# Optimization experiments

Hardware: AMD Instinct MI355X
Metric: run time of the kernel (lower is better)

Reference implementation:

```python
import jax, jax.numpy as jnp
import numpy as np

BS9 = 9
NA9 = BS9 * BS9  # 81


def _make_windows():
    """All 5-in-a-row windows on a 9x9 board, as flat cell indices. (140, 5)."""
    wins = []
    for dr, dc in ((0, 1), (1, 0), (1, 1), (1, -1)):
        for r in range(BS9):
            for c in range(BS9):
                er, ec = r + 4 * dr, c + 4 * dc
                if 0 <= er < BS9 and 0 <= ec < BS9:
                    wins.append([(r + k * dr) * BS9 + (c + k * dc) for k in range(5)])
    return np.asarray(wins, dtype=np.int32)

_W_NP = _make_windows()                      # (140, 5)
_M_NP = np.zeros((NA9, _W_NP.shape[0]), dtype=np.int32)
for w in range(_W_NP.shape[0]):
    _M_NP[_W_NP[w], w] = 1                   # MEMBER[idx, w] = 1 iff cell idx is in window w

WINDOWS = jnp.asarray(_W_NP)                 # (140, 5)
MEMBER = jnp.asarray(_M_NP)                  # (81, 140)
# score table indexed by stone count 0..5 (pc>=5 clamps to 5 since window len is 5)
TABLE = jnp.asarray([0.0, 5.0, 50.0, 500.0, 5000.0, 100000.0], dtype=jnp.float32)


def setup_inputs() -> dict:
    key = jax.random.key(0)
    k1, k2 = jax.random.split(key)
    B = 2048
    boards = jax.random.randint(k1, (B, NA9), 0, 3).astype(jnp.float32)   # cells in {0,1,2}
    current_player = jax.random.randint(k2, (B,), 1, 3).astype(jnp.int32) # {1,2}
    return {"boards": boards, "current_player": current_player}


def reference(boards, current_player):
    # boards: (B, 81) float32 with values {0,1,2}; current_player: (B,) int32 {1,2}
    player = current_player.astype(boards.dtype)[:, None, None]  # (B,1,1)
    opp = 3.0 - player
    cells = boards[:, WINDOWS]                                    # (B,140,5)
    pc = jnp.sum(cells == player, axis=-1)                        # (B,140) player count per window
    oc = jnp.sum(cells == opp, axis=-1)                           # (B,140) opponent count

    # static eval of the current board (used for the value head)
    plus = jnp.where((oc == 0) & (pc > 0), TABLE[pc], 0.0)
    minus = jnp.where((pc == 0) & (oc > 0), TABLE[oc], 0.0)
    ev = jnp.sum(plus - minus, axis=-1)                           # (B,)

    # 1-ply lookahead: placing player's stone at empty cell idx adds MEMBER[idx] to pc
    pc_new = pc[:, None, :] + MEMBER[None]                        # (B,81,140)
    win = jnp.any((MEMBER[None] == 1) & (pc_new == 5), axis=-1)   # (B,81)
    ocb = oc[:, None, :]
    plus_n = jnp.where((ocb == 0) & (pc_new > 0), TABLE[pc_new], 0.0)
    minus_n = jnp.where((pc_new == 0) & (ocb > 0), TABLE[ocb], 0.0)
    score = jnp.sum(plus_n - minus_n, axis=-1)                    # (B,81)

    empty = boards == 0                                           # (B,81)
    logits = jnp.where(empty, jnp.where(win, 100000.0, score), -1000000.0)
    policy = jax.nn.softmax(logits * 0.03, axis=-1)               # (B,81)
    value = jnp.clip(jnp.tanh(ev / 3000.0), -0.95, 0.95)[:, None] # (B,1)
    return policy, value
```

## Files before the change

kernel.cpp:

```cpp
#include <hip/hip_runtime.h>
#include <math.h>

#define NB 81
#define NW 140

struct Tables {
    unsigned long long mlo[NW];
    unsigned long long mhi[NW];
    unsigned cw32[NB][5];
};

constexpr Tables make_tables() {
    Tables t{};
    for (int a = 0; a < NB; ++a)
        for (int j = 0; j < 5; ++j) t.cw32[a][j] = 0x8C8C8C8Cu;
    int cnt[NB] = {};
    const int DR[4] = {0, 1, 1, 1};
    const int DC[4] = {1, 0, 1, -1};
    int w = 0;
    for (int d = 0; d < 4; ++d)
        for (int r = 0; r < 9; ++r)
            for (int c = 0; c < 9; ++c) {
                const int er = r + 4 * DR[d], ec = c + 4 * DC[d];
                if (er < 0 || er > 8 || ec < 0 || ec > 8) continue;
                unsigned long long lo = 0, hi = 0;
                for (int k = 0; k < 5; ++k) {
                    const int cell = (r + k * DR[d]) * 9 + (c + k * DC[d]);
                    if (cell < 64) lo |= 1ull << cell;
                    else           hi |= 1ull << (cell - 64);
                    const int i = cnt[cell]++;
                    t.cw32[cell][i >> 2] &= ~(0xFFu << (8 * (i & 3)));
                    t.cw32[cell][i >> 2] |= (unsigned)w << (8 * (i & 3));
                }
                t.mlo[w] = lo; t.mhi[w] = hi; ++w;
            }
    return t;
}

__device__ __constant__ Tables TAB = make_tables();
__device__ __constant__ float PT[6] = {0.f, 5.f, 50.f, 500.f, 5000.f, 100000.f};
__device__ __constant__ float DT[6] = {5.f, 45.f, 450.f, 4500.f, 95000.f, 0.f};

__device__ __forceinline__ float wave_sum(float v) {
#pragma unroll
    for (int m = 1; m < 64; m <<= 1) v += __shfl_xor(v, m, 64);
    return v;
}
__device__ __forceinline__ float wave_max(float v) {
#pragma unroll
    for (int m = 1; m < 64; m <<= 1) v = fmaxf(v, __shfl_xor(v, m, 64));
    return v;
}

__global__ __launch_bounds__(256) void heur9_kernel(const float* __restrict__ boards,
                                                    const int* __restrict__ cur,
                                                    float* __restrict__ out, int B) {
    __shared__ float sD[4][NW + 1];
    const int wave = threadIdx.x >> 6;
    const int lane = threadIdx.x & 63;
    const int b = (blockIdx.x << 2) | wave;
    float* dl = sD[wave];
    const float* brd = boards + b * NB;

    const float pf = (float)cur[b];
    const float of = 3.0f - pf;
    const float v1 = brd[lane];
    const float v2 = (lane < NB - 64) ? brd[lane + 64] : -1.0f;

    const unsigned long long p_lo = __ballot(v1 == pf);
    const unsigned long long p_hi = __ballot((lane < NB - 64) && v2 == pf);
    const unsigned long long o_lo = __ballot(v1 == of);
    const unsigned long long o_hi = __ballot((lane < NB - 64) && v2 == of);
    const unsigned long long e_lo = ~(p_lo | o_lo);
    const unsigned long long e_hi = ~(p_hi | o_hi);

    float evp = 0.f;
    for (int w = lane; w < NW; w += 64) {
        const int pc = __popcll(p_lo & TAB.mlo[w]) + __popcll(p_hi & TAB.mhi[w]);
        const int oc = __popcll(o_lo & TAB.mlo[w]) + __popcll(o_hi & TAB.mhi[w]);
        float d = 0.f;
        if (oc == 0)      { d = DT[pc]; evp += PT[pc]; }
        else if (pc == 0) { d = PT[oc]; evp -= PT[oc]; }
        if (pc == 4) d = 1.0e9f;
        dl[w] = d;
    }
    if (lane == 0) dl[NW] = 0.f;
    const float ev = wave_sum(evp);
    __syncthreads();

    float sd1 = 0.f, sd2 = 0.f;
#pragma unroll
    for (int j = 0; j < 5; ++j) {
        const unsigned q = TAB.cw32[lane][j];
        sd1 += dl[q & 255] + dl[(q >> 8) & 255] + dl[(q >> 16) & 255] + dl[q >> 24];
    }
    if (lane < NB - 64) {
#pragma unroll
        for (int j = 0; j < 5; ++j) {
            const unsigned q = TAB.cw32[lane + 64][j];
            sd2 += dl[q & 255] + dl[(q >> 8) & 255] + dl[(q >> 16) & 255] + dl[q >> 24];
        }
    }
    const bool emp1 = (e_lo >> lane) & 1ull;
    const bool emp2 = (lane < NB - 64) && ((e_hi >> lane) & 1ull);
    float l1 = emp1 ? (sd1 >= 5.0e8f ? 100000.f : ev + sd1) : -1000000.f;
    float l2 = (lane < NB - 64)
                 ? (emp2 ? (sd2 >= 5.0e8f ? 100000.f : ev + sd2) : -1000000.f)
                 : -INFINITY;
    l1 *= 0.03f; l2 *= 0.03f;

    const float m = wave_max(fmaxf(l1, l2));
    const float e1 = __expf(l1 - m);
    const float e2 = (lane < NB - 64) ? __expf(l2 - m) : 0.f;
    const float inv = 1.0f / wave_sum(e1 + e2);

    out[b * NB + lane] = e1 * inv;
    if (lane < NB - 64) out[b * NB + lane + 64] = e2 * inv;
    if (lane == 0) {
        const float v = tanhf(ev * (1.f / 3000.f));
        out[B * NB + b] = fminf(fmaxf(v, -0.95f), 0.95f);
    }
}

extern "C" void kernel_launch(void* const* d_in, const int* in_sizes, int n_in,
                              void* d_out, int out_size, void* d_ws, size_t ws_size,
                              hipStream_t stream) {
    const float* boards = (const float*)d_in[0];
    const int* cur = (const int*)d_in[1];
    float* out = (float*)d_out;
    const int B = in_sizes[0] / NB;
    heur9_kernel<<<B / 4, 256, 0, stream>>>(boards, cur, out, B);
}
```

Before: 57.75 us.

## Replace per-cell window gathers with per-line prefix sums over window deltas

Groups the 140 windows into 36 board lines and has each line lane compute a running prefix sum of window deltas in shared memory. Each cell's lookahead score then becomes four prefix-sum differences (one per direction) instead of gathering up to 20 window deltas. This cuts shared-memory reads per cell but serialises a 5-step scan on only 36 lanes. It also lowers the win sentinel to 2^21 so float prefix differences stay exact, which relies on the non-win deltas staying well below the 1e6 threshold.

```diff
diff --git a/kernel.cpp b/kernel.cpp
--- a/kernel.cpp
+++ b/kernel.cpp
@@ -3,37 +3,59 @@
 
 #define NB 81
 #define NW 140
+#define NL 36
+#define PSZ (NL * 6)
+#define WINM 2097152.0f
 
 struct Tables {
-    unsigned long long mlo[NW];
-    unsigned long long mhi[NW];
-    unsigned cw32[NB][5];
+    unsigned long long lmlo[NL][5];
+    unsigned long long lmhi[NL][5];
+    unsigned char len[NL];
+    unsigned cellPS[NB][2];
 };
 
 constexpr Tables make_tables() {
     Tables t{};
+    int minp[NB][4] = {}, maxp[NB][4] = {}, lofc[NB][4] = {};
     for (int a = 0; a < NB; ++a)
-        for (int j = 0; j < 5; ++j) t.cw32[a][j] = 0x8C8C8C8Cu;
-    int cnt[NB] = {};
+        for (int d = 0; d < 4; ++d) { minp[a][d] = 99; maxp[a][d] = -1; }
     const int DR[4] = {0, 1, 1, 1};
     const int DC[4] = {1, 0, 1, -1};
-    int w = 0;
     for (int d = 0; d < 4; ++d)
         for (int r = 0; r < 9; ++r)
             for (int c = 0; c < 9; ++c) {
                 const int er = r + 4 * DR[d], ec = c + 4 * DC[d];
                 if (er < 0 || er > 8 || ec < 0 || ec > 8) continue;
+                int l = 0;
+                if (d == 0) l = r;
+                else if (d == 1) l = 9 + c;
+                else if (d == 2) l = 18 + (r - c + 4);
+                else l = 27 + (r + c - 4);
+                const int pos = t.len[l]++;
                 unsigned long long lo = 0, hi = 0;
                 for (int k = 0; k < 5; ++k) {
                     const int cell = (r + k * DR[d]) * 9 + (c + k * DC[d]);
                     if (cell < 64) lo |= 1ull << cell;
                     else           hi |= 1ull << (cell - 64);
-                    const int i = cnt[cell]++;
-                    t.cw32[cell][i >> 2] &= ~(0xFFu << (8 * (i & 3)));
-                    t.cw32[cell][i >> 2] |= (unsigned)w << (8 * (i & 3));
+                    lofc[cell][d] = l;
+                    if (pos < minp[cell][d]) minp[cell][d] = pos;
+                    if (pos > maxp[cell][d]) maxp[cell][d] = pos;
                 }
-                t.mlo[w] = lo; t.mhi[w] = hi; ++w;
+                t.lmlo[l][pos] = lo; t.lmhi[l][pos] = hi;
             }
+    for (int a = 0; a < NB; ++a) {
+        unsigned q[2] = {0, 0};
+        for (int d = 0; d < 4; ++d) {
+            unsigned hiS = 0, loS = 0;
+            if (maxp[a][d] >= 0) {
+                const int l = lofc[a][d];
+                loS = (unsigned)(l * 6 + minp[a][d]);
+                hiS = (unsigned)(l * 6 + 1 + maxp[a][d]);
+            }
+            q[d >> 1] |= (hiS | (loS << 8)) << (16 * (d & 1));
+        }
+        t.cellPS[a][0] = q[0]; t.cellPS[a][1] = q[1];
+    }
     return t;
 }
 
@@ -55,11 +77,11 @@
 __global__ __launch_bounds__(256) void heur9_kernel(const float* __restrict__ boards,
                                                     const int* __restrict__ cur,
                                                     float* __restrict__ out, int B) {
-    __shared__ float sD[4][NW + 1];
+    __shared__ float sP[4][PSZ];
     const int wave = threadIdx.x >> 6;
     const int lane = threadIdx.x & 63;
     const int b = (blockIdx.x << 2) | wave;
-    float* dl = sD[wave];
+    float* P = sP[wave];
     const float* brd = boards + b * NB;
 
     const float pf = (float)cur[b];
@@ -75,37 +97,42 @@
     const unsigned long long e_hi = ~(p_hi | o_hi);
 
     float evp = 0.f;
-    for (int w = lane; w < NW; w += 64) {
-        const int pc = __popcll(p_lo & TAB.mlo[w]) + __popcll(p_hi & TAB.mhi[w]);
-        const int oc = __popcll(o_lo & TAB.mlo[w]) + __popcll(o_hi & TAB.mhi[w]);
-        float d = 0.f;
-        if (oc == 0)      { d = DT[pc]; evp += PT[pc]; }
-        else if (pc == 0) { d = PT[oc]; evp -= PT[oc]; }
-        if (pc == 4) d = 1.0e9f;
-        dl[w] = d;
+    if (lane < NL) {
+        const int len = TAB.len[lane];
+        float run = 0.f;
+        P[lane * 6] = 0.f;
+#pragma unroll
+        for (int pos = 0; pos < 5; ++pos) {
+            const unsigned long long ml = TAB.lmlo[lane][pos];
+            const unsigned long long mh = TAB.lmhi[lane][pos];
+            const int pc = __popcll(p_lo & ml) + __popcll(p_hi & mh);
+            const int oc = __popcll(o_lo & ml) + __popcll(o_hi & mh);
+            float d = 0.f;
+            if (oc == 0)      { d = DT[pc]; evp += PT[pc]; }
+            else if (pc == 0) { d = PT[oc]; evp -= PT[oc]; }
+            if (pc == 4) d = WINM;
+            if (pos >= len) d = 0.f;
+            run += d;
+            P[lane * 6 + 1 + pos] = run;
+        }
     }
-    if (lane == 0) dl[NW] = 0.f;
     const float ev = wave_sum(evp);
     __syncthreads();
 
-    float sd1 = 0.f, sd2 = 0.f;
-#pragma unroll
-    for (int j = 0; j < 5; ++j) {
-        const unsigned q = TAB.cw32[lane][j];
-        sd1 += dl[q & 255] + dl[(q >> 8) & 255] + dl[(q >> 16) & 255] + dl[q >> 24];
-    }
+    const unsigned a0 = TAB.cellPS[lane][0], a1 = TAB.cellPS[lane][1];
+    float sd1 = (P[a0 & 255] - P[(a0 >> 8) & 255]) + (P[(a0 >> 16) & 255] - P[a0 >> 24])
+              + (P[a1 & 255] - P[(a1 >> 8) & 255]) + (P[(a1 >> 16) & 255] - P[a1 >> 24]);
+    float sd2 = 0.f;
     if (lane < NB - 64) {
-#pragma unroll
-        for (int j = 0; j < 5; ++j) {
-            const unsigned q = TAB.cw32[lane + 64][j];
-            sd2 += dl[q & 255] + dl[(q >> 8) & 255] + dl[(q >> 16) & 255] + dl[q >> 24];
-        }
+        const unsigned b0 = TAB.cellPS[lane + 64][0], b1 = TAB.cellPS[lane + 64][1];
+        sd2 = (P[b0 & 255] - P[(b0 >> 8) & 255]) + (P[(b0 >> 16) & 255] - P[b0 >> 24])
+            + (P[b1 & 255] - P[(b1 >> 8) & 255]) + (P[(b1 >> 16) & 255] - P[b1 >> 24]);
     }
     const bool emp1 = (e_lo >> lane) & 1ull;
     const bool emp2 = (lane < NB - 64) && ((e_hi >> lane) & 1ull);
-    float l1 = emp1 ? (sd1 >= 5.0e8f ? 100000.f : ev + sd1) : -1000000.f;
+    float l1 = emp1 ? (sd1 >= 1.0e6f ? 100000.f : ev + sd1) : -1000000.f;
     float l2 = (lane < NB - 64)
-                 ? (emp2 ? (sd2 >= 5.0e8f ? 100000.f : ev + sd2) : -1000000.f)
+                 ? (emp2 ? (sd2 >= 1.0e6f ? 100000.f : ev + sd2) : -1000000.f)
                  : -INFINITY;
     l1 *= 0.03f; l2 *= 0.03f;
 
```

Measured after the change: 58.37 us. Within noise of the previous version (+1.1%).
